# Optimization experiments

Hardware: AMD Instinct MI355X
Metric: run time of the kernel (lower is better)

## Reference

```python
import jax, jax.numpy as jnp
import numpy as np

N = 500          # number of gaussians (hardcoded loop bound in source)
H = W = 1024     # fixed raster grid in source


def setup_inputs() -> dict:
    key = jax.random.key(0)
    k1, k2, k3 = jax.random.split(key, 3)
    # means in pixel coordinates
    mean = jax.random.uniform(k1, (N, 2), dtype=jnp.float32, minval=0.0, maxval=1023.0)
    # depth as produced by __init__: clamp(x/2.5 + 0.6, 0.1, 1) * 10  -> in [1, 10]
    depth = jnp.clip(jax.random.normal(k2, (N,), dtype=jnp.float32) / 2.5 + 0.6, 0.1, 1.0) * 10.0
    # radii is a log-std; scaled O(1) so splats cover multiple pixels
    radii = jnp.abs(jax.random.normal(k3, (N,), dtype=jnp.float32)) * 1.5 + 0.5
    # fixed red color per gaussian, as in __init__
    color = jnp.tile(jnp.array([255.0, 0.0, 0.0], dtype=jnp.float32), (N, 1))
    return {"mean": mean, "depth": depth, "radii": radii, "color": color}


def reference(mean, depth, radii, color):
    # torch.meshgrid default is 'ij' indexing
    xx, yy = jnp.meshgrid(jnp.arange(H, dtype=jnp.float32),
                          jnp.arange(W, dtype=jnp.float32), indexing="ij")
    two_pi = jnp.float32(2.0 * np.pi)

    def body(acc, p):
        m, d, r, c = p  # m:[2], d:[], r:[], c:[3]
        # rotated coords simplify: xx_rot - m0 = xx - yy + m1 - m0 ; yy_rot - m1 = xx + yy - m0 - m1
        u = xx - yy + (m[1] - m[0])
        v = xx + yy - (m[0] + m[1])
        inv_var = jnp.exp(-2.0 * r)  # 1 / exp(2*log_std)
        # normalizer uses exp(r/2)*exp(r/2) = exp(r) as in the source
        g = d * jnp.exp(-0.5 * (u * u + v * v) * inv_var) / (two_pi * jnp.exp(r))
        return acc + c[:, None, None] * g, None

    acc0 = jnp.zeros((3, H, W), dtype=jnp.float32)
    out, _ = jax.lax.scan(body, acc0, (mean, depth, radii, color))
    return out
```

## Files before the change

kernel.cpp:

```cpp
#include <hip/hip_runtime.h>
#include <math.h>

#define HH 1024
#define WW 1024
#define TW 32
#define TH 8
#define NTX (WW / TW)
#define NTY (HH / TH)
#define THREADS 256
#define MAXG 512


__global__ __launch_bounds__(256) void gauss_prep(
    const float* __restrict__ mean, const float* __restrict__ depth,
    const float* __restrict__ radii, const float* __restrict__ color,
    float* __restrict__ params, int n) {
  int g = blockIdx.x * blockDim.x + threadIdx.x;
  if (g >= n) return;
  float m0 = mean[2 * g + 0];
  float m1 = mean[2 * g + 1];
  float d  = depth[g];
  float r  = radii[g];

  const float LOG2E = 1.4426950408889634f;
  const float TWO_PI = 6.283185307179586f;

  float q = 0.5f * LOG2E * __expf(-2.0f * r);
  float s = sqrtf(q);
  float As  = (m1 - m0) * s;
  float Bsn = -(m0 + m1) * s;
  float norm = d / (TWO_PI * __expf(r));
  float w0 = color[3 * g + 0] * norm;
  float w1 = color[3 * g + 1] * norm;
  float w2 = color[3 * g + 2] * norm;
  float wmax = fmaxf(fabsf(w0), fmaxf(fabsf(w1), fabsf(w2)));
  float R2s = __log2f(wmax * 1e5f);

  float* p = params + 8 * g;
  p[0] = s;  p[1] = As; p[2] = Bsn; p[3] = R2s;
  p[4] = w0; p[5] = w1; p[6] = w2;  p[7] = 0.0f;
}

__global__ __launch_bounds__(THREADS) void gauss_raster(
    const float4* __restrict__ params, float* __restrict__ out, int n) {
  __shared__ int s_count;
  __shared__ int s_flag;
  __shared__ float4 s_pa[MAXG];
  __shared__ float2 s_pb[MAXG];

  const int tile_x = blockIdx.x % NTX;
  const int tile_y = blockIdx.x / NTX;
  const int j0 = tile_x * TW;
  const int i0 = tile_y * TH;

  if (threadIdx.x == 0) { s_count = 0; s_flag = 0; }
  __syncthreads();

  for (int g = threadIdx.x; g < n; g += THREADS) {
    float4 pa = params[2 * g + 0];
    float4 pb = params[2 * g + 1];
    float s = pa.x, As = pa.y, Bsn = pa.z, R2s = pa.w;
    float ul = fmaf(s, (float)(i0 - (j0 + TW - 1)), As);
    float uh = fmaf(s, (float)(i0 + TH - 1 - j0), As);
    float vl = fmaf(s, (float)(i0 + j0), Bsn);
    float vh = fmaf(s, (float)(i0 + TH - 1 + j0 + TW - 1), Bsn);
    float du = fmaxf(0.0f, fmaxf(ul, -uh));
    float dv = fmaxf(0.0f, fmaxf(vl, -vh));
    if (fmaf(du, du, dv * dv) <= R2s) {
      int idx = atomicAdd(&s_count, 1);
      if (idx < MAXG) {
        s_pa[idx] = make_float4(s, As, Bsn, pb.x);
        s_pb[idx] = make_float2(pb.y, pb.z);
        if (pb.y != 0.0f || pb.z != 0.0f) s_flag = 1;
      }
    }
  }
  __syncthreads();
  int cnt = s_count;
  if (cnt > MAXG) cnt = MAXG;
  const int rgb = s_flag;

  const int jj = threadIdx.x & (TW - 1);
  const int ii = threadIdx.x >> 5;
  const int i_glob = i0 + ii;
  const int j_glob = j0 + jj;
  const float t1 = (float)(i_glob - j_glob);
  const float t2 = (float)(i_glob + j_glob);

  float a0 = 0.0f, a1 = 0.0f, a2 = 0.0f;

  if (!rgb) {
#pragma unroll 4
    for (int k = 0; k < cnt; ++k) {
      float4 pa = s_pa[k];
      float u = fmaf(t1, pa.x, pa.y);
      float v = fmaf(t2, pa.x, pa.z);
      float t = fmaf(v, v, u * u);
      float e = __builtin_amdgcn_exp2f(-t);
      a0 = fmaf(pa.w, e, a0);
    }
  } else {
#pragma unroll 4
    for (int k = 0; k < cnt; ++k) {
      float4 pa = s_pa[k];
      float2 pb = s_pb[k];
      float u = fmaf(t1, pa.x, pa.y);
      float v = fmaf(t2, pa.x, pa.z);
      float t = fmaf(v, v, u * u);
      float e = __builtin_amdgcn_exp2f(-t);
      a0 = fmaf(pa.w, e, a0);
      a1 = fmaf(pb.x, e, a1);
      a2 = fmaf(pb.y, e, a2);
    }
  }

  const int base = i_glob * WW + j_glob;
  out[0 * (HH * WW) + base] = a0;
  out[1 * (HH * WW) + base] = a1;
  out[2 * (HH * WW) + base] = a2;
}

extern "C" void kernel_launch(void* const* d_in, const int* in_sizes, int n_in,
                              void* d_out, int out_size, void* d_ws, size_t ws_size,
                              hipStream_t stream) {
  const float* mean  = (const float*)d_in[0];
  const float* depth = (const float*)d_in[1];
  const float* radii = (const float*)d_in[2];
  const float* color = (const float*)d_in[3];
  float* out = (float*)d_out;
  float* params = (float*)d_ws;
  int n = in_sizes[1];

  gauss_prep<<<(n + 255) / 256, 256, 0, stream>>>(mean, depth, radii, color,
                                                  params, n);
  gauss_raster<<<dim3(NTX * NTY), THREADS, 0, stream>>>(
      (const float4*)params, out, n);
}
```

Baseline: 67.69 us.

## Fuse gaussian parameter prep into raster kernel and permute tile order

```diff
diff --git a/kernel.cpp b/kernel.cpp
--- a/kernel.cpp
+++ b/kernel.cpp
@@ -7,59 +7,48 @@
 #define TH 8
 #define NTX (WW / TW)
 #define NTY (HH / TH)
+#define NT  (NTX * NTY)
 #define THREADS 256
 #define MAXG 512
 
 
-__global__ __launch_bounds__(256) void gauss_prep(
+__global__ __launch_bounds__(THREADS) void gauss_fused(
     const float* __restrict__ mean, const float* __restrict__ depth,
     const float* __restrict__ radii, const float* __restrict__ color,
-    float* __restrict__ params, int n) {
-  int g = blockIdx.x * blockDim.x + threadIdx.x;
-  if (g >= n) return;
-  float m0 = mean[2 * g + 0];
-  float m1 = mean[2 * g + 1];
-  float d  = depth[g];
-  float r  = radii[g];
-
-  const float LOG2E = 1.4426950408889634f;
-  const float TWO_PI = 6.283185307179586f;
-
-  float q = 0.5f * LOG2E * __expf(-2.0f * r);
-  float s = sqrtf(q);
-  float As  = (m1 - m0) * s;
-  float Bsn = -(m0 + m1) * s;
-  float norm = d / (TWO_PI * __expf(r));
-  float w0 = color[3 * g + 0] * norm;
-  float w1 = color[3 * g + 1] * norm;
-  float w2 = color[3 * g + 2] * norm;
-  float wmax = fmaxf(fabsf(w0), fmaxf(fabsf(w1), fabsf(w2)));
-  float R2s = __log2f(wmax * 1e5f);
-
-  float* p = params + 8 * g;
-  p[0] = s;  p[1] = As; p[2] = Bsn; p[3] = R2s;
-  p[4] = w0; p[5] = w1; p[6] = w2;  p[7] = 0.0f;
-}
-
-__global__ __launch_bounds__(THREADS) void gauss_raster(
-    const float4* __restrict__ params, float* __restrict__ out, int n) {
+    float* __restrict__ out, int n) {
   __shared__ int s_count;
   __shared__ int s_flag;
   __shared__ float4 s_pa[MAXG];
   __shared__ float2 s_pb[MAXG];
 
-  const int tile_x = blockIdx.x % NTX;
-  const int tile_y = blockIdx.x / NTX;
-  const int j0 = tile_x * TW;
-  const int i0 = tile_y * TH;
+  const int tile = (blockIdx.x * 1597) & (NT - 1);
+  const int j0 = (tile & (NTX - 1)) * TW;
+  const int i0 = (tile >> 5) * TH;
 
   if (threadIdx.x == 0) { s_count = 0; s_flag = 0; }
   __syncthreads();
 
+  const float LOG2E = 1.4426950408889634f;
+  const float TWO_PI = 6.283185307179586f;
+
   for (int g = threadIdx.x; g < n; g += THREADS) {
-    float4 pa = params[2 * g + 0];
-    float4 pb = params[2 * g + 1];
-    float s = pa.x, As = pa.y, Bsn = pa.z, R2s = pa.w;
+    float m0 = mean[2 * g + 0];
+    float m1 = mean[2 * g + 1];
+    float d  = depth[g];
+    float r  = radii[g];
+    float c0 = color[3 * g + 0];
+    float c1 = color[3 * g + 1];
+    float c2 = color[3 * g + 2];
+
+    float q = 0.5f * LOG2E * __expf(-2.0f * r);
+    float s = sqrtf(q);
+    float As  = (m1 - m0) * s;
+    float Bsn = -(m0 + m1) * s;
+    float norm = d * __frcp_rn(TWO_PI * __expf(r));
+    float w0 = c0 * norm, w1 = c1 * norm, w2 = c2 * norm;
+    float wmax = fmaxf(fabsf(w0), fmaxf(fabsf(w1), fabsf(w2)));
+    float R2s = __log2f(wmax * 1e5f);
+
     float ul = fmaf(s, (float)(i0 - (j0 + TW - 1)), As);
     float uh = fmaf(s, (float)(i0 + TH - 1 - j0), As);
     float vl = fmaf(s, (float)(i0 + j0), Bsn);
@@ -69,9 +58,9 @@
     if (fmaf(du, du, dv * dv) <= R2s) {
       int idx = atomicAdd(&s_count, 1);
       if (idx < MAXG) {
-        s_pa[idx] = make_float4(s, As, Bsn, pb.x);
-        s_pb[idx] = make_float2(pb.y, pb.z);
-        if (pb.y != 0.0f || pb.z != 0.0f) s_flag = 1;
+        s_pa[idx] = make_float4(s, As, Bsn, w0);
+        s_pb[idx] = make_float2(w1, w2);
+        if (w1 != 0.0f || w2 != 0.0f) s_flag = 1;
       }
     }
   }
@@ -128,11 +117,8 @@
   const float* radii = (const float*)d_in[2];
   const float* color = (const float*)d_in[3];
   float* out = (float*)d_out;
-  float* params = (float*)d_ws;
   int n = in_sizes[1];
 
-  gauss_prep<<<(n + 255) / 256, 256, 0, stream>>>(mean, depth, radii, color,
-                                                  params, n);
-  gauss_raster<<<dim3(NTX * NTY), THREADS, 0, stream>>>(
-      (const float4*)params, out, n);
+  gauss_fused<<<dim3(NT), THREADS, 0, stream>>>(mean, depth, radii, color,
+                                                out, n);
 }
```

Result: no change. 68.68 us (+1.5%).
